# Optimization experiments

Hardware: AMD Instinct MI355X
Metric: run time of the kernel (lower is better)

Reference implementation:

```python
import jax, jax.numpy as jnp
import numpy as np
import math

B, S, E, H, L, FF = 32, 512, 256, 8, 4, 1024
DH = E // H
EPS = 1e-5


def layernorm(x):
    # nn.LayerNorm(elementwise_affine=False)
    m = jnp.mean(x, axis=-1, keepdims=True)
    v = jnp.mean((x - m) ** 2, axis=-1, keepdims=True)
    return (x - m) / jnp.sqrt(v + EPS)


def make_pos_embedding(e):
    vals = [math.sin(1 / 10000 ** ((i - 1) / e)) if i % 2 == 1
            else math.cos(i / 10000 ** ((i - 1) / e)) for i in range(e)]
    return jnp.asarray(np.array(vals, dtype=np.float32))


def setup_inputs() -> dict:
    key = jax.random.key(0)
    ks = jax.random.split(key, 8)
    sc = 0.02
    x = jax.random.normal(ks[0], (B, S, E), dtype=jnp.float32)
    Wq = jax.random.normal(ks[1], (L, H, DH, DH), dtype=jnp.float32) * sc
    Wk = jax.random.normal(ks[2], (L, H, DH, DH), dtype=jnp.float32) * sc
    Wv = jax.random.normal(ks[3], (L, H, DH, DH), dtype=jnp.float32) * sc
    W1 = jax.random.normal(ks[4], (L, E, FF), dtype=jnp.float32) * sc
    b1 = jnp.zeros((L, FF), dtype=jnp.float32)
    W2 = jax.random.normal(ks[5], (L, FF, E), dtype=jnp.float32) * sc
    b2 = jnp.zeros((L, E), dtype=jnp.float32)
    pos = make_pos_embedding(E)
    return {"x": x, "pos": pos, "Wq": Wq, "Wk": Wk, "Wv": Wv,
            "W1": W1, "b1": b1, "W2": W2, "b2": b2}


def encoder_layer(x, wq, wk, wv, w1, bb1, w2, bb2):
    xn = layernorm(x)
    xh = xn.reshape(B, S, H, DH)  # split embedding into per-head chunks
    q = jnp.einsum('bshd,hde->bhse', xh, wq)
    k = jnp.einsum('bshd,hde->bhse', xh, wk)
    v = jnp.einsum('bshd,hde->bhse', xh, wv)
    scores = jnp.einsum('bhsd,bhtd->bhst', q, k) / jnp.sqrt(jnp.float32(DH))
    a = jax.nn.softmax(scores, axis=-1)
    o = jnp.einsum('bhst,bhtd->bhsd', a, v)
    mha = o.transpose(0, 2, 1, 3).reshape(B, S, E)  # concat heads
    res = mha + x
    rn = layernorm(res)
    ffn = jax.nn.gelu(rn @ w1 + bb1, approximate=False) @ w2 + bb2
    return ffn + res


def reference(x, pos, Wq, Wk, Wv, W1, b1, W2, b2):
    h = x + pos  # fixed sinusoidal positional embedding
    for l in range(L):
        h = encoder_layer(h, Wq[l], Wk[l], Wv[l], W1[l], b1[l], W2[l], b2[l])
    return h
```

## Files before the change

kernel.cpp:

```cpp
#include <hip/hip_runtime.h>
#include <math.h>

#define BB   32
#define SS   512
#define EE   256
#define HH   8
#define LL   4
#define FFD  1024
#define DHD  32

constexpr float LN_EPS = 1e-5f;
constexpr int   NBSE   = BB * SS * EE;

typedef float  f32x4  __attribute__((ext_vector_type(4)));
typedef __bf16 bf16;
typedef __bf16 bf16x4 __attribute__((ext_vector_type(4)));
typedef __bf16 bf16x8 __attribute__((ext_vector_type(8)));

__device__ __forceinline__ void glds16(const bf16* g, bf16* l) {
    __builtin_amdgcn_global_load_lds(
        (const __attribute__((address_space(1))) void*)g,
        (__attribute__((address_space(3))) void*)l,
        16, 0, 0);
}

__device__ __forceinline__ float gelu_f(float x) {
    float u = x * x;
    float t = 1.5957691216057308f * x * (1.0f + 0.044715f * u);
    return x / (1.0f + __expf(-t));
}

__global__ __launch_bounds__(256) void k_cvt_t(const float* __restrict__ in,
                                               bf16* __restrict__ out,
                                               int K, int N) {
    __shared__ float tile[32][33];
    in  += (size_t)blockIdx.z * K * N;
    out += (size_t)blockIdx.z * K * N;
    int n0 = blockIdx.x * 32, k0 = blockIdx.y * 32;
    int tx = threadIdx.x & 31, ty = threadIdx.x >> 5;
    #pragma unroll
    for (int i = 0; i < 32; i += 8)
        tile[ty + i][tx] = in[(size_t)(k0 + ty + i) * N + n0 + tx];
    __syncthreads();
    #pragma unroll
    for (int i = 0; i < 32; i += 8)
        out[(size_t)(n0 + ty + i) * K + k0 + tx] = (bf16)tile[tx][ty + i];
}

__global__ __launch_bounds__(256) void k_cvt_qkv(const float* __restrict__ Wq,
                                                 const float* __restrict__ Wk,
                                                 const float* __restrict__ Wv,
                                                 bf16* __restrict__ Wqt,
                                                 bf16* __restrict__ Wkt,
                                                 bf16* __restrict__ Wvt) {
    __shared__ float tile[32][33];
    int lh = blockIdx.x;
    int z  = blockIdx.y;
    const float* in = (z == 0 ? Wq : z == 1 ? Wk : Wv) + (size_t)lh * 1024;
    bf16* out       = (z == 0 ? Wqt : z == 1 ? Wkt : Wvt) + (size_t)lh * 1024;
    float scale = (z == 0) ? 0.17677669529663687f : 1.0f;
    int tx = threadIdx.x & 31, ty = threadIdx.x >> 5;
    #pragma unroll
    for (int i = 0; i < 32; i += 8)
        tile[ty + i][tx] = in[(ty + i) * 32 + tx];
    __syncthreads();
    #pragma unroll
    for (int i = 0; i < 32; i += 8)
        out[(ty + i) * 32 + tx] = (bf16)(tile[tx][ty + i] * scale);
}

template <bool ADDPOS>
__global__ __launch_bounds__(256) void k_lnqkv(const float* __restrict__ xin,
                                               const float* __restrict__ pos,
                                               float* __restrict__ hout,
                                               const bf16* __restrict__ Wqt,
                                               const bf16* __restrict__ Wkt,
                                               const bf16* __restrict__ Wvt,
                                               bf16* __restrict__ qb,
                                               bf16* __restrict__ kb,
                                               bf16* __restrict__ vb) {
    __shared__ __attribute__((aligned(16))) bf16 Xs[64 * 264];
    int b = blockIdx.x, s0 = blockIdx.y * 64;
    int tid = threadIdx.x, w = tid >> 6, lane = tid & 63;
    size_t rowoff = ((size_t)(b * SS + s0 + w * 16)) * EE + lane * 4;
    const float* hb = xin + rowoff;
    float4 pv;
    if (ADDPOS) pv = *(const float4*)(pos + lane * 4);
    float4 xr[16];
    #pragma unroll
    for (int i = 0; i < 16; i++)
        xr[i] = *(const float4*)(hb + (size_t)i * EE);
    if (ADDPOS) {
        #pragma unroll
        for (int i = 0; i < 16; i++) {
            xr[i].x += pv.x; xr[i].y += pv.y; xr[i].z += pv.z; xr[i].w += pv.w;
            *(float4*)(hout + rowoff + (size_t)i * EE) = xr[i];
        }
    }
    #pragma unroll
    for (int i = 0; i < 16; i++) {
        float4 v4 = xr[i];
        float sum = v4.x + v4.y + v4.z + v4.w;
        #pragma unroll
        for (int m = 1; m <= 32; m <<= 1) sum += __shfl_xor(sum, m, 64);
        float mean = sum * (1.0f / EE);
        float dx = v4.x - mean, dy = v4.y - mean, dz = v4.z - mean, dw = v4.w - mean;
        float ss = dx * dx + dy * dy + dz * dz + dw * dw;
        #pragma unroll
        for (int m = 1; m <= 32; m <<= 1) ss += __shfl_xor(ss, m, 64);
        float rstd = rsqrtf(ss * (1.0f / EE) + LN_EPS);
        bf16x4 o4 = { (bf16)(dx * rstd), (bf16)(dy * rstd), (bf16)(dz * rstd), (bf16)(dw * rstd) };
        *(bf16x4*)&Xs[(w * 16 + i) * 264 + lane * 4] = o4;
    }
    __syncthreads();
    int col = lane & 15, quad = lane >> 4;
    #pragma unroll
    for (int h = 0; h < HH; h++) {
        bf16x8 a = *(const bf16x8*)&Xs[(w * 16 + col) * 264 + h * 32 + quad * 8];
        size_t base = ((size_t)((b * HH + h) * SS) + s0 + w * 16) * DHD;
        #pragma unroll
        for (int nt = 0; nt < 2; nt++) {
            int e = nt * 16 + col;
            bf16x8 bq  = *(const bf16x8*)(Wqt + (h * 32 + e) * 32 + quad * 8);
            bf16x8 bk2 = *(const bf16x8*)(Wkt + (h * 32 + e) * 32 + quad * 8);
            bf16x8 bv2 = *(const bf16x8*)(Wvt + (h * 32 + e) * 32 + quad * 8);
            f32x4 z = {0.f, 0.f, 0.f, 0.f};
            f32x4 cq = __builtin_amdgcn_mfma_f32_16x16x32_bf16(a, bq, z, 0, 0, 0);
            f32x4 ck = __builtin_amdgcn_mfma_f32_16x16x32_bf16(a, bk2, z, 0, 0, 0);
            f32x4 cv = __builtin_amdgcn_mfma_f32_16x16x32_bf16(a, bv2, z, 0, 0, 0);
            #pragma unroll
            for (int r = 0; r < 4; r++) {
                qb[base + (quad * 4 + r) * DHD + e] = (bf16)cq[r];
                kb[base + (quad * 4 + r) * DHD + e] = (bf16)ck[r];
            }
            bf16x4 vv = { (bf16)cv[0], (bf16)cv[1], (bf16)cv[2], (bf16)cv[3] };
            *(bf16x4*)&vb[(((size_t)(b * HH + h)) * DHD + e) * SS + s0 + w * 16 + quad * 4] = vv;
        }
    }
}

#define ATT_LDK 40
#define ATT_LDV 264
#define ATT_LDP 36
__global__ __launch_bounds__(256) void k_attn(const bf16* __restrict__ Q,
                                              const bf16* __restrict__ K,
                                              const bf16* __restrict__ VT,
                                              bf16* __restrict__ O) {
    __shared__ __attribute__((aligned(16))) bf16 Ks[256 * ATT_LDK];
    __shared__ __attribute__((aligned(16))) bf16 Vs[32 * ATT_LDV];
    __shared__ __attribute__((aligned(16))) bf16 Ps[4][16 * ATT_LDP];
    int bh = blockIdx.x;
    int q0 = blockIdx.y * 128;
    int tid = threadIdx.x;
    int w = tid >> 6, lane = tid & 63;
    int col = lane & 15, quad = lane >> 4;
    bf16x8 aq[2];
    #pragma unroll
    for (int sub = 0; sub < 2; sub++)
        aq[sub] = *(const bf16x8*)(Q + ((size_t)(bh * SS + q0 + sub * 64 + w * 16 + col)) * DHD + quad * 8);
    float lr[2] = {0.f, 0.f};
    f32x4 oacc[2][2] = {};
    int ksr = tid >> 2, ksc = (tid & 3) * 8;
    int vd  = tid >> 5, vso = (tid & 31) * 8;
    for (int ph = 0; ph < 2; ph++) {
        int t00 = ph * 256;
        __syncthreads();
        #pragma unroll
        for (int it = 0; it < 4; it++) {
            int rl = it * 64 + ksr;
            *(bf16x8*)&Ks[rl * ATT_LDK + ksc] =
                *(const bf16x8*)(K + ((size_t)(bh * SS + t00 + rl)) * DHD + ksc);
        }
        #pragma unroll
        for (int it = 0; it < 4; it++) {
            int d = it * 8 + vd;
            *(bf16x8*)&Vs[d * ATT_LDV + vso] =
                *(const bf16x8*)(VT + (((size_t)bh * DHD + d) * SS) + t00 + vso);
        }
        __syncthreads();
        #pragma unroll
        for (int i = 0; i < 8; i++) {
            bf16x8 bk[2], bv[2];
            #pragma unroll
            for (int nt = 0; nt < 2; nt++) {
                bk[nt] = *(const bf16x8*)&Ks[(i * 32 + nt * 16 + col) * ATT_LDK + quad * 8];
                bv[nt] = *(const bf16x8*)&Vs[(nt * 16 + col) * ATT_LDV + i * 32 + quad * 8];
            }
            #pragma unroll
            for (int sub = 0; sub < 2; sub++) {
                #pragma unroll
                for (int nt = 0; nt < 2; nt++) {
                    f32x4 z = {0.f, 0.f, 0.f, 0.f};
                    f32x4 st = __builtin_amdgcn_mfma_f32_16x16x32_bf16(bk[nt], aq[sub], z, 0, 0, 0);
                    bf16x4 p4;
                    #pragma unroll
                    for (int r = 0; r < 4; r++) {
                        float p = __expf(st[r]);
                        lr[sub] += p;
                        p4[r] = (bf16)p;
                    }
                    *(bf16x4*)&Ps[w][col * ATT_LDP + nt * 16 + quad * 4] = p4;
                }
                bf16x4 apl = *(const bf16x4*)&Ps[w][col * ATT_LDP + quad * 8];
                bf16x4 aph = *(const bf16x4*)&Ps[w][col * ATT_LDP + quad * 8 + 4];
                bf16x8 ap;
                ap[0] = apl[0]; ap[1] = apl[1]; ap[2] = apl[2]; ap[3] = apl[3];
                ap[4] = aph[0]; ap[5] = aph[1]; ap[6] = aph[2]; ap[7] = aph[3];
                #pragma unroll
                for (int nt = 0; nt < 2; nt++)
                    oacc[sub][nt] = __builtin_amdgcn_mfma_f32_16x16x32_bf16(ap, bv[nt], oacc[sub][nt], 0, 0, 0);
            }
        }
    }
    int b = bh >> 3, hh = bh & 7;
    #pragma unroll
    for (int sub = 0; sub < 2; sub++) {
        float ls = lr[sub];
        ls += __shfl_xor(ls, 16, 64);
        ls += __shfl_xor(ls, 32, 64);
        #pragma unroll
        for (int r = 0; r < 4; r++) {
            float lrow = __shfl(ls, quad * 4 + r, 64);
            float inv = 1.0f / lrow;
            int row = q0 + sub * 64 + w * 16 + quad * 4 + r;
            size_t ob = ((size_t)(b * SS + row)) * EE + hh * 32;
            O[ob + col]      = (bf16)(oacc[sub][0][r] * inv);
            O[ob + 16 + col] = (bf16)(oacc[sub][1][r] * inv);
        }
    }
}

__global__ __launch_bounds__(256) void k_resln(const bf16* __restrict__ ob,
                                               const float* __restrict__ hb,
                                               bf16* __restrict__ rn) {
    int row  = blockIdx.x * 4 + (threadIdx.x >> 6);
    int lane = threadIdx.x & 63;
    float4 h4 = *(const float4*)(hb + (size_t)row * EE + lane * 4);
    bf16x4 o4 = *(const bf16x4*)(ob + (size_t)row * EE + lane * 4);
    float v0 = h4.x + (float)o4[0], v1 = h4.y + (float)o4[1];
    float v2 = h4.z + (float)o4[2], v3 = h4.w + (float)o4[3];
    float sum = v0 + v1 + v2 + v3;
    #pragma unroll
    for (int m = 1; m <= 32; m <<= 1) sum += __shfl_xor(sum, m, 64);
    float mean = sum * (1.0f / EE);
    float d0 = v0 - mean, d1 = v1 - mean, d2 = v2 - mean, d3 = v3 - mean;
    float sq = d0 * d0 + d1 * d1 + d2 * d2 + d3 * d3;
    #pragma unroll
    for (int m = 1; m <= 32; m <<= 1) sq += __shfl_xor(sq, m, 64);
    float rstd = rsqrtf(sq * (1.0f / EE) + LN_EPS);
    bf16x4 r4 = { (bf16)(d0 * rstd), (bf16)(d1 * rstd), (bf16)(d2 * rstd), (bf16)(d3 * rstd) };
    *(bf16x4*)(rn + (size_t)row * EE + lane * 4) = r4;
}

__global__ __launch_bounds__(256) void k_gemm1(const bf16* __restrict__ A,
                                               const bf16* __restrict__ Bt,
                                               const float* __restrict__ bias,
                                               bf16* __restrict__ C) {
    __shared__ __attribute__((aligned(16))) bf16 As[128 * 32];
    __shared__ __attribute__((aligned(16))) bf16 Bs[128 * 32];
    int tid = threadIdx.x, w = tid >> 6, lane = tid & 63;
    int col = lane & 15, quad = lane >> 4;
    int wrow = w >> 1, wcol = w & 1;
    int row0 = blockIdx.x * 128, col0 = blockIdx.y * 128;
    int lrow = lane >> 2, lch = (lane & 3) * 8;
    const bf16* Ag = A  + (size_t)(row0 + w * 32 + lrow) * EE + lch;
    const bf16* Bg = Bt + (size_t)(col0 + w * 32 + lrow) * EE + lch;
    bf16* Asw = &As[(w * 32) * 32];
    bf16* Bsw = &Bs[(w * 32) * 32];
    f32x4 acc[4][4] = {};
    for (int k0 = 0; k0 < EE; k0 += 32) {
        glds16(Ag + k0, Asw);
        glds16(Ag + 16 * EE + k0, Asw + 16 * 32);
        glds16(Bg + k0, Bsw);
        glds16(Bg + 16 * EE + k0, Bsw + 16 * 32);
        __syncthreads();
        bf16x8 af[4], bf_[4];
        #pragma unroll
        for (int mt = 0; mt < 4; mt++)
            af[mt] = *(const bf16x8*)&As[(wrow * 64 + mt * 16 + col) * 32 + quad * 8];
        #pragma unroll
        for (int nt = 0; nt < 4; nt++)
            bf_[nt] = *(const bf16x8*)&Bs[(wcol * 64 + nt * 16 + col) * 32 + quad * 8];
        #pragma unroll
        for (int mt = 0; mt < 4; mt++)
            #pragma unroll
            for (int nt = 0; nt < 4; nt++)
                acc[mt][nt] = __builtin_amdgcn_mfma_f32_16x16x32_bf16(bf_[nt], af[mt], acc[mt][nt], 0, 0, 0);
        __syncthreads();
    }
    #pragma unroll
    for (int mt = 0; mt < 4; mt++) {
        int row = row0 + wrow * 64 + mt * 16 + col;
        #pragma unroll
        for (int nt = 0; nt < 4; nt++) {
            int cc = col0 + wcol * 64 + nt * 16 + quad * 4;
            float4 b4 = *(const float4*)&bias[cc];
            bf16x4 ov;
            ov[0] = (bf16)gelu_f(acc[mt][nt][0] + b4.x);
            ov[1] = (bf16)gelu_f(acc[mt][nt][1] + b4.y);
            ov[2] = (bf16)gelu_f(acc[mt][nt][2] + b4.z);
            ov[3] = (bf16)gelu_f(acc[mt][nt][3] + b4.w);
            *(bf16x4*)&C[(size_t)row * FFD + cc] = ov;
        }
    }
}

__global__ __launch_bounds__(256) void k_gemm2(const bf16* __restrict__ A,
                                               const bf16* __restrict__ Bt,
                                               const float* __restrict__ bias,
                                               const bf16* __restrict__ ob,
                                               const float* __restrict__ hb,
                                               float* __restrict__ Cf) {
    __shared__ __attribute__((aligned(16))) bf16 As[128 * 32];
    __shared__ __attribute__((aligned(16))) bf16 Bs[64 * 32];
    int tid = threadIdx.x, w = tid >> 6, lane = tid & 63;
    int col = lane & 15, quad = lane >> 4;
    int row0 = blockIdx.x * 128, col0 = blockIdx.y * 64;
    int lrow = lane >> 2, lch = (lane & 3) * 8;
    const bf16* Ag = A  + (size_t)(row0 + w * 32 + lrow) * FFD + lch;
    const bf16* Bg = Bt + (size_t)(col0 + w * 16 + lrow) * FFD + lch;
    bf16* Asw = &As[(w * 32) * 32];
    bf16* Bsw = &Bs[(w * 16) * 32];
    f32x4 acc[2][4] = {};
    for (int k0 = 0; k0 < FFD; k0 += 32) {
        glds16(Ag + k0, Asw);
        glds16(Ag + 16 * FFD + k0, Asw + 16 * 32);
        glds16(Bg + k0, Bsw);
        __syncthreads();
        bf16x8 af[2], bf_[4];
        #pragma unroll
        for (int mt = 0; mt < 2; mt++)
            af[mt] = *(const bf16x8*)&As[(w * 32 + mt * 16 + col) * 32 + quad * 8];
        #pragma unroll
        for (int nt = 0; nt < 4; nt++)
            bf_[nt] = *(const bf16x8*)&Bs[(nt * 16 + col) * 32 + quad * 8];
        #pragma unroll
        for (int mt = 0; mt < 2; mt++)
            #pragma unroll
            for (int nt = 0; nt < 4; nt++)
                acc[mt][nt] = __builtin_amdgcn_mfma_f32_16x16x32_bf16(bf_[nt], af[mt], acc[mt][nt], 0, 0, 0);
        __syncthreads();
    }
    #pragma unroll
    for (int mt = 0; mt < 2; mt++) {
        int row = row0 + w * 32 + mt * 16 + col;
        #pragma unroll
        for (int nt = 0; nt < 4; nt++) {
            int cc = col0 + nt * 16 + quad * 4;
            float4 b4 = *(const float4*)&bias[cc];
            float4 h4 = *(const float4*)&hb[(size_t)row * EE + cc];
            bf16x4 o4 = *(const bf16x4*)&ob[(size_t)row * EE + cc];
            float4 out;
            out.x = acc[mt][nt][0] + b4.x + h4.x + (float)o4[0];
            out.y = acc[mt][nt][1] + b4.y + h4.y + (float)o4[1];
            out.z = acc[mt][nt][2] + b4.z + h4.z + (float)o4[2];
            out.w = acc[mt][nt][3] + b4.w + h4.w + (float)o4[3];
            *(float4*)&Cf[(size_t)row * EE + cc] = out;
        }
    }
}

extern "C" void kernel_launch(void* const* d_in, const int* in_sizes, int n_in,
                              void* d_out, int out_size, void* d_ws, size_t ws_size,
                              hipStream_t stream) {
    (void)in_sizes; (void)n_in; (void)out_size; (void)ws_size;
    const float* x   = (const float*)d_in[0];
    const float* pos = (const float*)d_in[1];
    const float* Wq  = (const float*)d_in[2];
    const float* Wk  = (const float*)d_in[3];
    const float* Wv  = (const float*)d_in[4];
    const float* W1  = (const float*)d_in[5];
    const float* b1  = (const float*)d_in[6];
    const float* W2  = (const float*)d_in[7];
    const float* b2  = (const float*)d_in[8];

    float* ws = (float*)d_ws;
    size_t N = (size_t)NBSE;
    float* h  = ws;
    bf16* ob  = (bf16*)(ws + N);
    bf16* rnb = (bf16*)(ws + N) + N;
    bf16* qb  = (bf16*)(ws + 2 * N);
    bf16* kb  = qb + N;
    bf16* vb  = kb + N;
    bf16* ffb = (bf16*)(ws + 2 * N);
    bf16* W1t = (bf16*)(ws + 4 * N);
    bf16* W2t = W1t + (size_t)LL * EE * FFD;
    bf16* Wqt = W2t + (size_t)LL * EE * FFD;
    bf16* Wkt = Wqt + (size_t)LL * HH * DHD * DHD;
    bf16* Wvt = Wkt + (size_t)LL * HH * DHD * DHD;

    k_cvt_t<<<dim3(FFD / 32, EE / 32, LL), 256, 0, stream>>>(W1, W1t, EE, FFD);
    k_cvt_t<<<dim3(EE / 32, FFD / 32, LL), 256, 0, stream>>>(W2, W2t, FFD, EE);
    k_cvt_qkv<<<dim3(LL * HH, 3), 256, 0, stream>>>(Wq, Wk, Wv, Wqt, Wkt, Wvt);
    for (int l = 0; l < LL; l++) {
        if (l == 0)
            k_lnqkv<true><<<dim3(BB, SS / 64), 256, 0, stream>>>(
                x, pos, h, Wqt, Wkt, Wvt, qb, kb, vb);
        else
            k_lnqkv<false><<<dim3(BB, SS / 64), 256, 0, stream>>>(
                h, nullptr, nullptr,
                Wqt + (size_t)l * HH * DHD * DHD, Wkt + (size_t)l * HH * DHD * DHD,
                Wvt + (size_t)l * HH * DHD * DHD, qb, kb, vb);
        k_attn<<<dim3(BB * HH, SS / 128), 256, 0, stream>>>(qb, kb, vb, ob);
        k_resln<<<BB * SS / 4, 256, 0, stream>>>(ob, h, rnb);
        k_gemm1<<<dim3(BB * SS / 128, FFD / 128), 256, 0, stream>>>(
            rnb, W1t + (size_t)l * FFD * EE, b1 + (size_t)l * FFD, ffb);
        float* outp = (l == LL - 1) ? (float*)d_out : h;
        k_gemm2<<<dim3(BB * SS / 128, EE / 64), 256, 0, stream>>>(
            ffb, W2t + (size_t)l * EE * FFD, b2 + (size_t)l * EE, ob, h, outp);
    }
}
```

Baseline: 459.8 us.

## Fuse residual LayerNorm, FFN up-projection, GELU and down-projection into one kernel

Replaces the separate resln, gemm1 and gemm2 kernels with a single k_ffn kernel. Each 64-row block normalizes its rows into LDS, computes the hidden activation in 128-wide chunks with GELU into LDS, and accumulates the second GEMM directly. This avoids writing and re-reading the 32 MB bf16 intermediate and the normalized activations, and removes two launches. Weights are now read straight from global memory without LDS staging, and every block re-reads the full W1 and W2, which may become cache-bound or latency-bound.

```diff
diff --git a/kernel.cpp b/kernel.cpp
--- a/kernel.cpp
+++ b/kernel.cpp
@@ -8,6 +8,7 @@
 #define LL   4
 #define FFD  1024
 #define DHD  32
+#define FCH  128
 
 constexpr float LN_EPS = 1e-5f;
 constexpr int   NBSE   = BB * SS * EE;
@@ -16,13 +17,6 @@
 typedef __bf16 bf16;
 typedef __bf16 bf16x4 __attribute__((ext_vector_type(4)));
 typedef __bf16 bf16x8 __attribute__((ext_vector_type(8)));
-
-__device__ __forceinline__ void glds16(const bf16* g, bf16* l) {
-    __builtin_amdgcn_global_load_lds(
-        (const __attribute__((address_space(1))) void*)g,
-        (__attribute__((address_space(3))) void*)l,
-        16, 0, 0);
-}
 
 __device__ __forceinline__ float gelu_f(float x) {
     float u = x * x;
@@ -230,132 +224,107 @@
     }
 }
 
-__global__ __launch_bounds__(256) void k_resln(const bf16* __restrict__ ob,
-                                               const float* __restrict__ hb,
-                                               bf16* __restrict__ rn) {
-    int row  = blockIdx.x * 4 + (threadIdx.x >> 6);
-    int lane = threadIdx.x & 63;
-    float4 h4 = *(const float4*)(hb + (size_t)row * EE + lane * 4);
-    bf16x4 o4 = *(const bf16x4*)(ob + (size_t)row * EE + lane * 4);
-    float v0 = h4.x + (float)o4[0], v1 = h4.y + (float)o4[1];
-    float v2 = h4.z + (float)o4[2], v3 = h4.w + (float)o4[3];
-    float sum = v0 + v1 + v2 + v3;
-    #pragma unroll
-    for (int m = 1; m <= 32; m <<= 1) sum += __shfl_xor(sum, m, 64);
-    float mean = sum * (1.0f / EE);
-    float d0 = v0 - mean, d1 = v1 - mean, d2 = v2 - mean, d3 = v3 - mean;
-    float sq = d0 * d0 + d1 * d1 + d2 * d2 + d3 * d3;
-    #pragma unroll
-    for (int m = 1; m <= 32; m <<= 1) sq += __shfl_xor(sq, m, 64);
-    float rstd = rsqrtf(sq * (1.0f / EE) + LN_EPS);
-    bf16x4 r4 = { (bf16)(d0 * rstd), (bf16)(d1 * rstd), (bf16)(d2 * rstd), (bf16)(d3 * rstd) };
-    *(bf16x4*)(rn + (size_t)row * EE + lane * 4) = r4;
-}
-
-__global__ __launch_bounds__(256) void k_gemm1(const bf16* __restrict__ A,
-                                               const bf16* __restrict__ Bt,
-                                               const float* __restrict__ bias,
-                                               bf16* __restrict__ C) {
-    __shared__ __attribute__((aligned(16))) bf16 As[128 * 32];
-    __shared__ __attribute__((aligned(16))) bf16 Bs[128 * 32];
+__global__ __launch_bounds__(512, 2) void k_ffn(const bf16* __restrict__ ob,
+                                                const float* __restrict__ hb,
+                                                const bf16* __restrict__ W1t,
+                                                const float* __restrict__ b1,
+                                                const bf16* __restrict__ W2t,
+                                                const float* __restrict__ b2,
+                                                float* __restrict__ out) {
+    __shared__ __attribute__((aligned(16))) bf16 As[64 * 264];
+    __shared__ __attribute__((aligned(16))) bf16 Ps[64 * 136];
     int tid = threadIdx.x, w = tid >> 6, lane = tid & 63;
     int col = lane & 15, quad = lane >> 4;
-    int wrow = w >> 1, wcol = w & 1;
-    int row0 = blockIdx.x * 128, col0 = blockIdx.y * 128;
-    int lrow = lane >> 2, lch = (lane & 3) * 8;
-    const bf16* Ag = A  + (size_t)(row0 + w * 32 + lrow) * EE + lch;
-    const bf16* Bg = Bt + (size_t)(col0 + w * 32 + lrow) * EE + lch;
-    bf16* Asw = &As[(w * 32) * 32];
-    bf16* Bsw = &Bs[(w * 32) * 32];
-    f32x4 acc[4][4] = {};
-    for (int k0 = 0; k0 < EE; k0 += 32) {
-        glds16(Ag + k0, Asw);
-        glds16(Ag + 16 * EE + k0, Asw + 16 * 32);
-        glds16(Bg + k0, Bsw);
-        glds16(Bg + 16 * EE + k0, Bsw + 16 * 32);
+    int row0 = blockIdx.x * 64;
+    #pragma unroll
+    for (int i = 0; i < 8; i++) {
+        int r = w * 8 + i;
+        float4 h4 = *(const float4*)(hb + (size_t)(row0 + r) * EE + lane * 4);
+        bf16x4 o4 = *(const bf16x4*)(ob + (size_t)(row0 + r) * EE + lane * 4);
+        float v0 = h4.x + (float)o4[0], v1 = h4.y + (float)o4[1];
+        float v2 = h4.z + (float)o4[2], v3 = h4.w + (float)o4[3];
+        float sum = v0 + v1 + v2 + v3;
+        #pragma unroll
+        for (int m = 1; m <= 32; m <<= 1) sum += __shfl_xor(sum, m, 64);
+        float mean = sum * (1.0f / EE);
+        float d0 = v0 - mean, d1 = v1 - mean, d2 = v2 - mean, d3 = v3 - mean;
+        float sq = d0 * d0 + d1 * d1 + d2 * d2 + d3 * d3;
+        #pragma unroll
+        for (int m = 1; m <= 32; m <<= 1) sq += __shfl_xor(sq, m, 64);
+        float rstd = rsqrtf(sq * (1.0f / EE) + LN_EPS);
+        bf16x4 a4 = { (bf16)(d0 * rstd), (bf16)(d1 * rstd), (bf16)(d2 * rstd), (bf16)(d3 * rstd) };
+        *(bf16x4*)&As[r * 264 + lane * 4] = a4;
+    }
+    __syncthreads();
+    int mrow  = (w >> 2) * 32;
+    int ncol1 = (w & 3) * 32;
+    int ncol2 = (w & 3) * 64;
+    bf16x8 af[2][8];
+    #pragma unroll
+    for (int mt = 0; mt < 2; mt++)
+        #pragma unroll
+        for (int s = 0; s < 8; s++)
+            af[mt][s] = *(const bf16x8*)&As[(mrow + mt * 16 + col) * 264 + s * 32 + quad * 8];
+    f32x4 accF[2][4] = {};
+    for (int c = 0; c < 8; c++) {
+        f32x4 accC[2][2] = {};
+        #pragma unroll
+        for (int s = 0; s < 8; s++) {
+            #pragma unroll
+            for (int nt = 0; nt < 2; nt++) {
+                bf16x8 bfv = *(const bf16x8*)(W1t +
+                    (size_t)(c * FCH + ncol1 + nt * 16 + col) * EE + s * 32 + quad * 8);
+                #pragma unroll
+                for (int mt = 0; mt < 2; mt++)
+                    accC[mt][nt] = __builtin_amdgcn_mfma_f32_16x16x32_bf16(bfv, af[mt][s], accC[mt][nt], 0, 0, 0);
+            }
+        }
+        #pragma unroll
+        for (int mt = 0; mt < 2; mt++)
+            #pragma unroll
+            for (int nt = 0; nt < 2; nt++) {
+                int ccl = ncol1 + nt * 16 + quad * 4;
+                float4 b4 = *(const float4*)&b1[c * FCH + ccl];
+                bf16x4 p4;
+                p4[0] = (bf16)gelu_f(accC[mt][nt][0] + b4.x);
+                p4[1] = (bf16)gelu_f(accC[mt][nt][1] + b4.y);
+                p4[2] = (bf16)gelu_f(accC[mt][nt][2] + b4.z);
+                p4[3] = (bf16)gelu_f(accC[mt][nt][3] + b4.w);
+                *(bf16x4*)&Ps[(mrow + mt * 16 + col) * 136 + ccl] = p4;
+            }
         __syncthreads();
-        bf16x8 af[4], bf_[4];
-        #pragma unroll
-        for (int mt = 0; mt < 4; mt++)
-            af[mt] = *(const bf16x8*)&As[(wrow * 64 + mt * 16 + col) * 32 + quad * 8];
-        #pragma unroll
-        for (int nt = 0; nt < 4; nt++)
-            bf_[nt] = *(const bf16x8*)&Bs[(wcol * 64 + nt * 16 + col) * 32 + quad * 8];
-        #pragma unroll
-        for (int mt = 0; mt < 4; mt++)
-            #pragma unroll
-            for (int nt = 0; nt < 4; nt++)
-                acc[mt][nt] = __builtin_amdgcn_mfma_f32_16x16x32_bf16(bf_[nt], af[mt], acc[mt][nt], 0, 0, 0);
+        #pragma unroll
+        for (int s2 = 0; s2 < 4; s2++) {
+            bf16x8 ap[2];
+            #pragma unroll
+            for (int mt = 0; mt < 2; mt++)
+                ap[mt] = *(const bf16x8*)&Ps[(mrow + mt * 16 + col) * 136 + s2 * 32 + quad * 8];
+            #pragma unroll
+            for (int nt = 0; nt < 4; nt++) {
+                bf16x8 bw = *(const bf16x8*)(W2t +
+                    (size_t)(ncol2 + nt * 16 + col) * FFD + c * FCH + s2 * 32 + quad * 8);
+                #pragma unroll
+                for (int mt = 0; mt < 2; mt++)
+                    accF[mt][nt] = __builtin_amdgcn_mfma_f32_16x16x32_bf16(bw, ap[mt], accF[mt][nt], 0, 0, 0);
+            }
+        }
         __syncthreads();
     }
     #pragma unroll
-    for (int mt = 0; mt < 4; mt++) {
-        int row = row0 + wrow * 64 + mt * 16 + col;
+    for (int mt = 0; mt < 2; mt++) {
+        int row = row0 + mrow + mt * 16 + col;
         #pragma unroll
         for (int nt = 0; nt < 4; nt++) {
-            int cc = col0 + wcol * 64 + nt * 16 + quad * 4;
-            float4 b4 = *(const float4*)&bias[cc];
-            bf16x4 ov;
-            ov[0] = (bf16)gelu_f(acc[mt][nt][0] + b4.x);
-            ov[1] = (bf16)gelu_f(acc[mt][nt][1] + b4.y);
-            ov[2] = (bf16)gelu_f(acc[mt][nt][2] + b4.z);
-            ov[3] = (bf16)gelu_f(acc[mt][nt][3] + b4.w);
-            *(bf16x4*)&C[(size_t)row * FFD + cc] = ov;
-        }
-    }
-}
-
-__global__ __launch_bounds__(256) void k_gemm2(const bf16* __restrict__ A,
-                                               const bf16* __restrict__ Bt,
-                                               const float* __restrict__ bias,
-                                               const bf16* __restrict__ ob,
-                                               const float* __restrict__ hb,
-                                               float* __restrict__ Cf) {
-    __shared__ __attribute__((aligned(16))) bf16 As[128 * 32];
-    __shared__ __attribute__((aligned(16))) bf16 Bs[64 * 32];
-    int tid = threadIdx.x, w = tid >> 6, lane = tid & 63;
-    int col = lane & 15, quad = lane >> 4;
-    int row0 = blockIdx.x * 128, col0 = blockIdx.y * 64;
-    int lrow = lane >> 2, lch = (lane & 3) * 8;
-    const bf16* Ag = A  + (size_t)(row0 + w * 32 + lrow) * FFD + lch;
-    const bf16* Bg = Bt + (size_t)(col0 + w * 16 + lrow) * FFD + lch;
-    bf16* Asw = &As[(w * 32) * 32];
-    bf16* Bsw = &Bs[(w * 16) * 32];
-    f32x4 acc[2][4] = {};
-    for (int k0 = 0; k0 < FFD; k0 += 32) {
-        glds16(Ag + k0, Asw);
-        glds16(Ag + 16 * FFD + k0, Asw + 16 * 32);
-        glds16(Bg + k0, Bsw);
-        __syncthreads();
-        bf16x8 af[2], bf_[4];
-        #pragma unroll
-        for (int mt = 0; mt < 2; mt++)
-            af[mt] = *(const bf16x8*)&As[(w * 32 + mt * 16 + col) * 32 + quad * 8];
-        #pragma unroll
-        for (int nt = 0; nt < 4; nt++)
-            bf_[nt] = *(const bf16x8*)&Bs[(nt * 16 + col) * 32 + quad * 8];
-        #pragma unroll
-        for (int mt = 0; mt < 2; mt++)
-            #pragma unroll
-            for (int nt = 0; nt < 4; nt++)
-                acc[mt][nt] = __builtin_amdgcn_mfma_f32_16x16x32_bf16(bf_[nt], af[mt], acc[mt][nt], 0, 0, 0);
-        __syncthreads();
-    }
-    #pragma unroll
-    for (int mt = 0; mt < 2; mt++) {
-        int row = row0 + w * 32 + mt * 16 + col;
-        #pragma unroll
-        for (int nt = 0; nt < 4; nt++) {
-            int cc = col0 + nt * 16 + quad * 4;
-            float4 b4 = *(const float4*)&bias[cc];
+            int cc = ncol2 + nt * 16 + quad * 4;
+            float4 b4 = *(const float4*)&b2[cc];
             float4 h4 = *(const float4*)&hb[(size_t)row * EE + cc];
             bf16x4 o4 = *(const bf16x4*)&ob[(size_t)row * EE + cc];
-            float4 out;
-            out.x = acc[mt][nt][0] + b4.x + h4.x + (float)o4[0];
-            out.y = acc[mt][nt][1] + b4.y + h4.y + (float)o4[1];
-            out.z = acc[mt][nt][2] + b4.z + h4.z + (float)o4[2];
-            out.w = acc[mt][nt][3] + b4.w + h4.w + (float)o4[3];
-            *(float4*)&Cf[(size_t)row * EE + cc] = out;
+            float4 o;
+            o.x = accF[mt][nt][0] + b4.x + h4.x + (float)o4[0];
+            o.y = accF[mt][nt][1] + b4.y + h4.y + (float)o4[1];
+            o.z = accF[mt][nt][2] + b4.z + h4.z + (float)o4[2];
+            o.w = accF[mt][nt][3] + b4.w + h4.w + (float)o4[3];
+            *(float4*)&out[(size_t)row * EE + cc] = o;
         }
     }
 }
@@ -378,11 +347,9 @@
     size_t N = (size_t)NBSE;
     float* h  = ws;
     bf16* ob  = (bf16*)(ws + N);
-    bf16* rnb = (bf16*)(ws + N) + N;
     bf16* qb  = (bf16*)(ws + 2 * N);
     bf16* kb  = qb + N;
     bf16* vb  = kb + N;
-    bf16* ffb = (bf16*)(ws + 2 * N);
     bf16* W1t = (bf16*)(ws + 4 * N);
     bf16* W2t = W1t + (size_t)LL * EE * FFD;
     bf16* Wqt = W2t + (size_t)LL * EE * FFD;
@@ -402,11 +369,9 @@
                 Wqt + (size_t)l * HH * DHD * DHD, Wkt + (size_t)l * HH * DHD * DHD,
                 Wvt + (size_t)l * HH * DHD * DHD, qb, kb, vb);
         k_attn<<<dim3(BB * HH, SS / 128), 256, 0, stream>>>(qb, kb, vb, ob);
-        k_resln<<<BB * SS / 4, 256, 0, stream>>>(ob, h, rnb);
-        k_gemm1<<<dim3(BB * SS / 128, FFD / 128), 256, 0, stream>>>(
-            rnb, W1t + (size_t)l * FFD * EE, b1 + (size_t)l * FFD, ffb);
         float* outp = (l == LL - 1) ? (float*)d_out : h;
-        k_gemm2<<<dim3(BB * SS / 128, EE / 64), 256, 0, stream>>>(
-            ffb, W2t + (size_t)l * EE * FFD, b2 + (size_t)l * EE, ob, h, outp);
-    }
-}
+        k_ffn<<<BB * SS / 64, 512, 0, stream>>>(
+            ob, h, W1t + (size_t)l * FFD * EE, b1 + (size_t)l * FFD,
+            W2t + (size_t)l * EE * FFD, b2 + (size_t)l * EE, outp);
+    }
+}
```

Measured after the change: 590.0 us. 28.3% more time.

## Fuse residual add and layernorm into the first FFN GEMM prologue

Applied to the files above, without the earlier changes.

Removes the separate residual+layernorm kernel and its bf16 intermediate buffer. The first FFN GEMM now computes the normalized residual for a 64-row slab directly into shared memory and keeps the full K=256 A-tile resident in registers, streaming only W1 tiles. Each 64-row slab is recomputed by all 8 column blocks, which adds redundant LN work and reads of h/ob. The tile also shrinks from 128x128 to 64x128, so each block does less MFMA work per loaded B tile.

```diff
diff --git a/kernel.cpp b/kernel.cpp
--- a/kernel.cpp
+++ b/kernel.cpp
@@ -230,70 +230,69 @@
     }
 }
 
-__global__ __launch_bounds__(256) void k_resln(const bf16* __restrict__ ob,
-                                               const float* __restrict__ hb,
-                                               bf16* __restrict__ rn) {
-    int row  = blockIdx.x * 4 + (threadIdx.x >> 6);
-    int lane = threadIdx.x & 63;
-    float4 h4 = *(const float4*)(hb + (size_t)row * EE + lane * 4);
-    bf16x4 o4 = *(const bf16x4*)(ob + (size_t)row * EE + lane * 4);
-    float v0 = h4.x + (float)o4[0], v1 = h4.y + (float)o4[1];
-    float v2 = h4.z + (float)o4[2], v3 = h4.w + (float)o4[3];
-    float sum = v0 + v1 + v2 + v3;
-    #pragma unroll
-    for (int m = 1; m <= 32; m <<= 1) sum += __shfl_xor(sum, m, 64);
-    float mean = sum * (1.0f / EE);
-    float d0 = v0 - mean, d1 = v1 - mean, d2 = v2 - mean, d3 = v3 - mean;
-    float sq = d0 * d0 + d1 * d1 + d2 * d2 + d3 * d3;
-    #pragma unroll
-    for (int m = 1; m <= 32; m <<= 1) sq += __shfl_xor(sq, m, 64);
-    float rstd = rsqrtf(sq * (1.0f / EE) + LN_EPS);
-    bf16x4 r4 = { (bf16)(d0 * rstd), (bf16)(d1 * rstd), (bf16)(d2 * rstd), (bf16)(d3 * rstd) };
-    *(bf16x4*)(rn + (size_t)row * EE + lane * 4) = r4;
-}
-
-__global__ __launch_bounds__(256) void k_gemm1(const bf16* __restrict__ A,
-                                               const bf16* __restrict__ Bt,
-                                               const float* __restrict__ bias,
-                                               bf16* __restrict__ C) {
-    __shared__ __attribute__((aligned(16))) bf16 As[128 * 32];
+__global__ __launch_bounds__(256) void k_gemm1n(const bf16* __restrict__ ob,
+                                                const float* __restrict__ hb,
+                                                const bf16* __restrict__ Bt,
+                                                const float* __restrict__ bias,
+                                                bf16* __restrict__ C) {
+    __shared__ __attribute__((aligned(16))) bf16 As[64 * 264];
     __shared__ __attribute__((aligned(16))) bf16 Bs[128 * 32];
     int tid = threadIdx.x, w = tid >> 6, lane = tid & 63;
     int col = lane & 15, quad = lane >> 4;
-    int wrow = w >> 1, wcol = w & 1;
-    int row0 = blockIdx.x * 128, col0 = blockIdx.y * 128;
+    int col0 = blockIdx.x * 128, row0 = blockIdx.y * 64;
+    #pragma unroll
+    for (int i = 0; i < 16; i++) {
+        int r = w * 16 + i;
+        float4 h4 = *(const float4*)(hb + (size_t)(row0 + r) * EE + lane * 4);
+        bf16x4 o4 = *(const bf16x4*)(ob + (size_t)(row0 + r) * EE + lane * 4);
+        float v0 = h4.x + (float)o4[0], v1 = h4.y + (float)o4[1];
+        float v2 = h4.z + (float)o4[2], v3 = h4.w + (float)o4[3];
+        float sum = v0 + v1 + v2 + v3;
+        #pragma unroll
+        for (int m = 1; m <= 32; m <<= 1) sum += __shfl_xor(sum, m, 64);
+        float mean = sum * (1.0f / EE);
+        float d0 = v0 - mean, d1 = v1 - mean, d2 = v2 - mean, d3 = v3 - mean;
+        float sq = d0 * d0 + d1 * d1 + d2 * d2 + d3 * d3;
+        #pragma unroll
+        for (int m = 1; m <= 32; m <<= 1) sq += __shfl_xor(sq, m, 64);
+        float rstd = rsqrtf(sq * (1.0f / EE) + LN_EPS);
+        bf16x4 a4 = { (bf16)(d0 * rstd), (bf16)(d1 * rstd), (bf16)(d2 * rstd), (bf16)(d3 * rstd) };
+        *(bf16x4*)&As[r * 264 + lane * 4] = a4;
+    }
+    __syncthreads();
+    int wrow = (w >> 1) * 32, wcol = (w & 1) * 64;
+    bf16x8 af[2][8];
+    #pragma unroll
+    for (int mt = 0; mt < 2; mt++)
+        #pragma unroll
+        for (int s = 0; s < 8; s++)
+            af[mt][s] = *(const bf16x8*)&As[(wrow + mt * 16 + col) * 264 + s * 32 + quad * 8];
     int lrow = lane >> 2, lch = (lane & 3) * 8;
-    const bf16* Ag = A  + (size_t)(row0 + w * 32 + lrow) * EE + lch;
     const bf16* Bg = Bt + (size_t)(col0 + w * 32 + lrow) * EE + lch;
-    bf16* Asw = &As[(w * 32) * 32];
     bf16* Bsw = &Bs[(w * 32) * 32];
-    f32x4 acc[4][4] = {};
+    f32x4 acc[2][4] = {};
     for (int k0 = 0; k0 < EE; k0 += 32) {
-        glds16(Ag + k0, Asw);
-        glds16(Ag + 16 * EE + k0, Asw + 16 * 32);
         glds16(Bg + k0, Bsw);
         glds16(Bg + 16 * EE + k0, Bsw + 16 * 32);
         __syncthreads();
-        bf16x8 af[4], bf_[4];
-        #pragma unroll
-        for (int mt = 0; mt < 4; mt++)
-            af[mt] = *(const bf16x8*)&As[(wrow * 64 + mt * 16 + col) * 32 + quad * 8];
+        bf16x8 bf_[4];
         #pragma unroll
         for (int nt = 0; nt < 4; nt++)
-            bf_[nt] = *(const bf16x8*)&Bs[(wcol * 64 + nt * 16 + col) * 32 + quad * 8];
-        #pragma unroll
-        for (int mt = 0; mt < 4; mt++)
+            bf_[nt] = *(const bf16x8*)&Bs[(wcol + nt * 16 + col) * 32 + quad * 8];
+        int s = k0 >> 5;
+        #pragma unroll
+        for (int mt = 0; mt < 2; mt++)
             #pragma unroll
             for (int nt = 0; nt < 4; nt++)
-                acc[mt][nt] = __builtin_amdgcn_mfma_f32_16x16x32_bf16(bf_[nt], af[mt], acc[mt][nt], 0, 0, 0);
-        __syncthreads();
-    }
-    #pragma unroll
-    for (int mt = 0; mt < 4; mt++) {
-        int row = row0 + wrow * 64 + mt * 16 + col;
+                acc[mt][nt] = __builtin_amdgcn_mfma_f32_16x16x32_bf16(bf_[nt], af[mt][s], acc[mt][nt], 0, 0, 0);
+        __syncthreads();
+    }
+    #pragma unroll
+    for (int mt = 0; mt < 2; mt++) {
+        int row = row0 + wrow + mt * 16 + col;
         #pragma unroll
         for (int nt = 0; nt < 4; nt++) {
-            int cc = col0 + wcol * 64 + nt * 16 + quad * 4;
+            int cc = col0 + wcol + nt * 16 + quad * 4;
             float4 b4 = *(const float4*)&bias[cc];
             bf16x4 ov;
             ov[0] = (bf16)gelu_f(acc[mt][nt][0] + b4.x);
@@ -378,7 +377,6 @@
     size_t N = (size_t)NBSE;
     float* h  = ws;
     bf16* ob  = (bf16*)(ws + N);
-    bf16* rnb = (bf16*)(ws + N) + N;
     bf16* qb  = (bf16*)(ws + 2 * N);
     bf16* kb  = qb + N;
     bf16* vb  = kb + N;
@@ -402,9 +400,8 @@
                 Wqt + (size_t)l * HH * DHD * DHD, Wkt + (size_t)l * HH * DHD * DHD,
                 Wvt + (size_t)l * HH * DHD * DHD, qb, kb, vb);
         k_attn<<<dim3(BB * HH, SS / 128), 256, 0, stream>>>(qb, kb, vb, ob);
-        k_resln<<<BB * SS / 4, 256, 0, stream>>>(ob, h, rnb);
-        k_gemm1<<<dim3(BB * SS / 128, FFD / 128), 256, 0, stream>>>(
-            rnb, W1t + (size_t)l * FFD * EE, b1 + (size_t)l * FFD, ffb);
+        k_gemm1n<<<dim3(FFD / 128, BB * SS / 64), 256, 0, stream>>>(
+            ob, h, W1t + (size_t)l * FFD * EE, b1 + (size_t)l * FFD, ffb);
         float* outp = (l == LL - 1) ? (float*)d_out : h;
         k_gemm2<<<dim3(BB * SS / 128, EE / 64), 256, 0, stream>>>(
             ffb, W2t + (size_t)l * EE * FFD, b2 + (size_t)l * EE, ob, h, outp);
```

New measurement: 535.8 us. +16.5%, slower.
